# Kernel optimization log

Hardware: AMD Instinct MI355X
Metric: run time of the kernel (lower is better)

The kernel has to match this reference:

```python
import jax, jax.numpy as jnp
import numpy as np

B, NT, DIM, HEADS = 8, 16, 768, 8
RES_H = RES_W = 32
PIX = RES_H * RES_W              # 1024
CHAN_NH = 16
NH = NW = 4                      # sqrt(chan_nheads)
WH, WW = RES_H // NH, RES_W // NW  # 8, 8
HEAD_DIM = DIM // HEADS          # 96
CHAN_HEAD_DIM = PIX // CHAN_NH   # 64


def _linear(x, w, b=None):
    y = x @ w.T
    return y if b is None else y + b


def _quat_kernel(r, i, j, k):
    # Hamilton-product block kernel: (4*out_c, 4*in_c, K)
    row_r = jnp.concatenate([r, -i, -j, -k], axis=1)
    row_i = jnp.concatenate([i, r, -k, j], axis=1)
    row_j = jnp.concatenate([j, k, r, -i], axis=1)
    row_k = jnp.concatenate([k, -j, i, r], axis=1)
    return jnp.concatenate([row_r, row_i, row_j, row_k], axis=0)


def _conv1d(x, w, b=None, pad=1):
    y = jax.lax.conv_general_dilated(x, w, (1,), [(pad, pad)],
                                     dimension_numbers=('NCH', 'OIH', 'NCH'))
    return y if b is None else y + b[None, :, None]


def _win(z, t):
    # 'b t (nh h nw w) -> b (nh nw) t (h w)'
    b = z.shape[0]
    z = z.reshape(b, t, NH, WH, NW, WW).transpose(0, 2, 4, 1, 3, 5)
    return z.reshape(b, NH * NW, t, WH * WW)


def setup_inputs():
    key = jax.random.key(0)
    ks = jax.random.split(key, 24)
    s = lambda i, shape: jax.random.normal(ks[i], shape, dtype=jnp.float32) * 0.02
    return dict(
        x=jax.random.normal(ks[0], (B, PIX, DIM), jnp.float32),
        task_prompts=jax.random.normal(ks[1], (B, NT, DIM), jnp.float32),
        qkv_w=s(2, (3 * DIM, DIM)),
        proj_w=s(3, (DIM, DIM)), proj_b=s(4, (DIM,)),
        tt_w=s(5, (PIX, DIM)), tt_b=s(6, (PIX,)),
        tt1_w=s(7, (DIM, PIX)), tt1_b=s(8, (DIM,)),
        qf_r=s(9, (2, 1, 3)), qf_i=s(10, (2, 1, 3)), qf_j=s(11, (2, 1, 3)),
        qf_k=s(12, (2, 1, 3)), qf_b=s(13, (8,)),
        dqf_r=s(14, (2, 1, 3)), dqf_i=s(15, (2, 1, 3)), dqf_j=s(16, (2, 1, 3)),
        dqf_k=s(17, (2, 1, 3)), dqf_b=s(18, (4,)),
        bn_g=jnp.ones((4,), jnp.float32), bn_b=jnp.zeros((4,), jnp.float32),
        qfto_w=s(19, (1, 4, 1)),
    )


def reference(x, task_prompts, qkv_w, proj_w, proj_b, tt_w, tt_b, tt1_w, tt1_b,
              qf_r, qf_i, qf_j, qf_k, qf_b, dqf_r, dqf_i, dqf_j, dqf_k, dqf_b,
              bn_g, bn_b, qfto_w):
    # ---- spatial attention over [prompts ; pixels] ----
    xc = jnp.concatenate([task_prompts, x], axis=1)           # (B, N, C), N = NT + PIX
    b, n, c = xc.shape
    qkv = _linear(xc, qkv_w).reshape(b, n, 3, HEADS, HEAD_DIM).transpose(2, 0, 3, 1, 4)
    q, k, v = qkv[0], qkv[1], qkv[2]
    raw_spa = jnp.einsum('bhqd,bhkd->bhqk', q, k)             # pre-scale logits (returned)
    spa_attn = jax.nn.softmax(raw_spa * HEAD_DIM ** -0.5, axis=-1)
    out = jnp.einsum('bhqk,bhkd->bhqd', spa_attn, v).transpose(0, 2, 1, 3).reshape(b, n, c)
    out = _linear(out, proj_w, proj_b)
    tp_out, x_out = out[:, :-PIX, :], out[:, -PIX:, :]        # sep_prompt(x, -pixel_no)

    # ---- windowed channel attention ----
    chan_x = x[:, -PIX:, :]                                   # (B, PIX, C)
    chan_prompts = _linear(task_prompts, tt_w, tt_b)          # (B, NT, PIX)
    qw = _win(chan_prompts, NT)                               # (B, 16, NT, 64)
    kw = _win(chan_x.transpose(0, 2, 1), DIM)                 # (B, 16, C, 64)
    raw_chan = jnp.einsum('bwtd,bwcd->bwtc', qw, kw)          # (B, 16, NT, C)
    chan_attn = jax.nn.softmax(raw_chan * CHAN_HEAD_DIM ** -0.5, axis=-1)
    # chan_x output of attn@v is computed in torch but unused downstream; XLA DCEs it.
    raw_chan_r = raw_chan.reshape(b, NH, NW, NT, DIM).transpose(0, 3, 4, 1, 2)   # b t c nh nw
    chan_attn_r = chan_attn.reshape(b, NH, NW, NT, DIM).transpose(0, 3, 4, 1, 2)

    # ---- quaternion fusion of prompt streams (vectorized over the torch per-sample loop) ----
    ch_prompts = _linear(chan_prompts, tt1_w, tt1_b)          # (B, NT, C)
    zero = jnp.zeros_like(tp_out)
    quater = jnp.stack([zero, task_prompts, tp_out, ch_prompts], axis=2)  # (B, NT, 4, C)
    w1 = _quat_kernel(qf_r, qf_i, qf_j, qf_k)                 # (8, 4, 3), OIH
    fe = _conv1d(quater.reshape(b * NT, 4, DIM), w1, qf_b)    # (B*NT, 8, C)
    w2 = _quat_kernel(dqf_r, dqf_i, dqf_j, dqf_k)             # (8, 4, 3) as (in, out, K)
    w2c = jnp.flip(w2, -1).transpose(1, 0, 2)                 # conv_transpose1d(s=1,p=1) == conv1d(flip, p=K-1-1)
    fe = _conv1d(fe, w2c, dqf_b).reshape(b, NT, 4, DIM)       # (B, NT, 4, C)
    # BatchNorm1d(4) in training mode, stats per loop iteration => per-sample over (NT, C)
    mean = fe.mean(axis=(1, 3), keepdims=True)
    var = fe.var(axis=(1, 3), keepdims=True)
    fe = (fe - mean) / jnp.sqrt(var + 1e-5) * bn_g[None, None, :, None] + bn_b[None, None, :, None]
    fe = jax.nn.gelu(fe, approximate=False)
    quater_out = jnp.einsum('bnkc,k->bnc', fe, qfto_w[0, :, 0])  # Conv1d(4,1,k=1,no bias)
    return (x_out, raw_spa, spa_attn, raw_chan_r, chan_attn_r, quater_out)
```

## Files before the change

### kernel.cpp

```cpp
#include <hip/hip_runtime.h>
#include <hip/hip_bf16.h>
#include <math.h>

typedef unsigned short u16;
typedef __attribute__((ext_vector_type(8))) short  bf16x8;
typedef __attribute__((ext_vector_type(4))) float  f32x4;
typedef __attribute__((ext_vector_type(8))) u16    u16x8;
typedef __attribute__((ext_vector_type(4))) u16    u16x4;

#define B_      8
#define NT_     16
#define DIM_    768
#define HEADS_  8
#define HD_     96
#define PIX_    1024
#define NTOK_   1040
#define NPAD_   1152

#define WSO_XCB     0ull
#define WSO_WQKV    12779520ull
#define WSO_WPROJ   16318464ull
#define WSO_QB      17498112ull
#define WSO_KB      31653888ull
#define WSO_VB      45809664ull
#define WSO_VTB     59965440ull
#define WSO_ACATB   74121216ull
#define WSO_TPB     86900736ull
#define WSO_TTWB    87097344ull
#define WSO_TT1WB   88670208ull
#define WSO_CHANPB  90243072ull
#define WSO_PART    90505216ull
#define WSO_F32     95813632ull
#define FO_TPOUT    0ull
#define FO_RAWCHAN  98304ull
#define FO_CHP      1671168ull
#define FO_FE2      1769472ull
#define FO_STATS    2162688ull

#define OUT_XOUT   0ull
#define OUT_RAW    6291456ull
#define OUT_ATTN   75513856ull
#define OUT_RAWCH  144736256ull
#define OUT_ATTNCH 146309120ull
#define OUT_QOUT   147881984ull

#define SCALE_SPA 0.1020620726159658f

__device__ __forceinline__ u16 f2b(float f) {
    union { float f; unsigned u; } x; x.f = f;
    unsigned r = x.u + 0x7FFFu + ((x.u >> 16) & 1u);
    return (u16)(r >> 16);
}
__device__ __forceinline__ u16 f2b_fast(float f) {
    __hip_bfloat16 h = __float2bfloat16(f);
    return __builtin_bit_cast(u16, h);
}
__device__ __forceinline__ float b2f(u16 h) {
    union { unsigned u; float f; } x; x.u = ((unsigned)h) << 16;
    return x.f;
}

__global__ __launch_bounds__(256) void cast_concat(const float* __restrict__ tp,
                                                   const float* __restrict__ x,
                                                   u16* __restrict__ xcb) {
    size_t idx8 = ((size_t)blockIdx.x * 256 + threadIdx.x) * 8;
    int c = idx8 % DIM_;
    int n = (idx8 / DIM_) % NTOK_;
    int b = idx8 / ((size_t)DIM_ * NTOK_);
    const float* s = (n < NT_) ? tp + ((size_t)b * NT_ + n) * DIM_ + c
                               : x + ((size_t)b * PIX_ + (n - NT_)) * DIM_ + c;
    float4 a = *(const float4*)s;
    float4 d = *(const float4*)(s + 4);
    u16x8 r;
    r[0] = f2b(a.x); r[1] = f2b(a.y); r[2] = f2b(a.z); r[3] = f2b(a.w);
    r[4] = f2b(d.x); r[5] = f2b(d.y); r[6] = f2b(d.z); r[7] = f2b(d.w);
    *(u16x8*)(xcb + idx8) = r;
}

__global__ __launch_bounds__(256) void cast_all(const float* __restrict__ qkv_w,
                                                const float* __restrict__ proj_w,
                                                const float* __restrict__ tp,
                                                const float* __restrict__ tt_w,
                                                const float* __restrict__ tt1_w,
                                                u16* __restrict__ wqkvb,
                                                u16* __restrict__ wprojb,
                                                u16* __restrict__ tpb,
                                                u16* __restrict__ ttwb,
                                                u16* __restrict__ tt1wb) {
    int i = blockIdx.x * 256 + threadIdx.x;
    const float* src;
    u16* dst;
    int li;
    if (i < 221184)      { src = qkv_w;  dst = wqkvb;  li = i; }
    else if (i < 294912) { src = proj_w; dst = wprojb; li = i - 221184; }
    else if (i < 307200) { src = tp;     dst = tpb;    li = i - 294912; }
    else if (i < 405504) { src = tt_w;   dst = ttwb;   li = i - 307200; }
    else if (i < 503808) { src = tt1_w;  dst = tt1wb;  li = i - 405504; }
    else return;
    const float* s = src + (size_t)li * 8;
    float4 a = *(const float4*)s;
    float4 d = *(const float4*)(s + 4);
    u16x8 r;
    r[0] = f2b(a.x); r[1] = f2b(a.y); r[2] = f2b(a.z); r[3] = f2b(a.w);
    r[4] = f2b(d.x); r[5] = f2b(d.y); r[6] = f2b(d.z); r[7] = f2b(d.w);
    *(u16x8*)(dst + (size_t)li * 8) = r;
}

template <int MODE>
__global__ __launch_bounds__(256) void gemm_bf16(
    const u16* __restrict__ A, const u16* __restrict__ Bw,
    int lda, int ldb, int K, size_t strA, size_t strB,
    const float* __restrict__ bias,
    float* __restrict__ o0, float* __restrict__ o1,
    u16* __restrict__ oq, u16* __restrict__ ok, u16* __restrict__ ov,
    int ldo) {
    __shared__ u16 As[128][40];
    __shared__ u16 Bs[128][40];
    __shared__ float redm[128][2];
    __shared__ float reds[128][2];
    const int tid = threadIdx.x;
    const int bm = blockIdx.x, bn = blockIdx.y, z = blockIdx.z;
    const u16* Ab = A + strA * z;
    const u16* Bb = Bw + strB * z;
    const int lane = tid & 63, wid = tid >> 6;
    const int ln = lane & 15, hi = lane >> 4;
    const int wr = wid >> 1, wc = wid & 1;
    const int srow = tid >> 1, scol = (tid & 1) * 16;
    f32x4 acc[4][4] = {};
    for (int kt = 0; kt < K; kt += 32) {
        __syncthreads();
        const u16* ga = Ab + (size_t)(bm * 128 + srow) * lda + kt + scol;
        const u16* gb = Bb + (size_t)(bn * 128 + srow) * ldb + kt + scol;
        u16x8 a0 = *(const u16x8*)ga, a1 = *(const u16x8*)(ga + 8);
        u16x8 b0 = *(const u16x8*)gb, b1 = *(const u16x8*)(gb + 8);
        *(u16x8*)&As[srow][scol] = a0;
        *(u16x8*)&As[srow][scol + 8] = a1;
        *(u16x8*)&Bs[srow][scol] = b0;
        *(u16x8*)&Bs[srow][scol + 8] = b1;
        __syncthreads();
        bf16x8 af[4], bfr[4];
#pragma unroll
        for (int m = 0; m < 4; ++m) af[m] = *(const bf16x8*)&As[wr * 64 + m * 16 + ln][hi * 8];
#pragma unroll
        for (int n = 0; n < 4; ++n) bfr[n] = *(const bf16x8*)&Bs[wc * 64 + n * 16 + ln][hi * 8];
#pragma unroll
        for (int m = 0; m < 4; ++m)
#pragma unroll
            for (int n = 0; n < 4; ++n)
                acc[m][n] = __builtin_amdgcn_mfma_f32_16x16x32_bf16(af[m], bfr[n], acc[m][n], 0, 0, 0);
    }
#pragma unroll
    for (int m = 0; m < 4; ++m) {
#pragma unroll
        for (int n = 0; n < 4; ++n) {
#pragma unroll
            for (int j = 0; j < 4; ++j) {
                int gm = bm * 128 + wr * 64 + m * 16 + hi * 4 + j;
                int gn = bn * 128 + wc * 64 + n * 16 + ln;
                float v = acc[m][n][j];
                if (MODE == 0) {
                    int b = gm / NTOK_, nn = gm - b * NTOK_;
                    int s = gn / DIM_, rem = gn - s * DIM_;
                    int h = rem / HD_, d = rem - h * HD_;
                    u16 hv = f2b(v);
                    u16* dst = (s == 0) ? oq : (s == 1) ? ok : ov;
                    dst[(((size_t)b * HEADS_ + h) * NPAD_ + nn) * HD_ + d] = hv;
                } else if (MODE == 1) {
                    if (gm < NTOK_ && gn < NTOK_)
                        o0[((size_t)z * NTOK_ + gm) * NTOK_ + gn] = v;
                } else if (MODE == 2) {
                    v += bias[gn];
                    int b = gm / NTOK_, nn = gm - b * NTOK_;
                    if (nn < NT_) o1[((size_t)b * NT_ + nn) * DIM_ + gn] = v;
                    else          o0[((size_t)b * PIX_ + (nn - NT_)) * DIM_ + gn] = v;
                } else if (MODE == 3) {
                    oq[(size_t)gm * ldo + gn] = f2b(v + bias[gn]);
                } else {
                    o0[(size_t)gm * ldo + gn] = v + bias[gn];
                }
            }
        }
    }
    if (MODE == 1) {
#pragma unroll
        for (int m = 0; m < 4; ++m) {
#pragma unroll
            for (int j = 0; j < 4; ++j) {
                float v[4];
                float mx = -INFINITY;
#pragma unroll
                for (int n = 0; n < 4; ++n) {
                    int gn = bn * 128 + wc * 64 + n * 16 + ln;
                    v[n] = (gn < NTOK_) ? acc[m][n][j] * SCALE_SPA : -INFINITY;
                    mx = fmaxf(mx, v[n]);
                }
#pragma unroll
                for (int off = 1; off < 16; off <<= 1) mx = fmaxf(mx, __shfl_xor(mx, off));
                float s = 0.f;
                if (mx > -INFINITY) {
#pragma unroll
                    for (int n = 0; n < 4; ++n)
                        if (v[n] > -INFINITY) s += __expf(v[n] - mx);
                }
#pragma unroll
                for (int off = 1; off < 16; off <<= 1) s += __shfl_xor(s, off);
                if (ln == 0) {
                    int row = wr * 64 + m * 16 + hi * 4 + j;
                    redm[row][wc] = mx;
                    reds[row][wc] = s;
                }
            }
        }
        __syncthreads();
        if (tid < 128) {
            float m0 = redm[tid][0], m1 = redm[tid][1];
            float s0 = reds[tid][0], s1 = reds[tid][1];
            float M = fmaxf(m0, m1);
            float S = 0.f;
            if (m0 > -INFINITY) S += s0 * __expf(m0 - M);
            if (m1 > -INFINITY) S += s1 * __expf(m1 - M);
            float2* pp = (float2*)o1;
            pp[((size_t)z * 9 + bn) * NPAD_ + bm * 128 + tid] = make_float2(M, S);
        }
    }
}

__global__ __launch_bounds__(256) void transpose_v(const u16* __restrict__ vb,
                                                   u16* __restrict__ vtb) {
    __shared__ u16 t[32][34];
    int bi = blockIdx.x, bj = blockIdx.y, z = blockIdx.z;
    const u16* ib = vb + (size_t)z * NPAD_ * HD_;
    u16* ob = vtb + (size_t)z * HD_ * NPAD_;
    int tid = threadIdx.x;
    int r = tid >> 3, c = (tid & 7) * 4;
    *(u16x4*)&t[r][c] = *(const u16x4*)(ib + (size_t)(bi * 32 + r) * HD_ + bj * 32 + c);
    __syncthreads();
    u16x4 o;
    o[0] = t[c + 0][r]; o[1] = t[c + 1][r]; o[2] = t[c + 2][r]; o[3] = t[c + 3][r];
    *(u16x4*)(ob + (size_t)(bj * 32 + r) * NPAD_ + bi * 32 + c) = o;
}

__global__ __launch_bounds__(256) void attn_pv3(const float* __restrict__ raw,
                                                const float2* __restrict__ part,
                                                const u16* __restrict__ vtb,
                                                float* __restrict__ attn,
                                                u16* __restrict__ acat) {
    __shared__ u16 Ps[32][136];
    __shared__ float sm[32], si[32];
    const int tid = threadIdx.x;
    const int bi = blockIdx.x, z = blockIdx.y;
    if (tid < 32) {
        int grow = bi * 32 + tid;
        float M = -INFINITY;
        float mj[9], sj[9];
#pragma unroll
        for (int jt = 0; jt < 9; ++jt) {
            float2 p = part[((size_t)z * 9 + jt) * NPAD_ + grow];
            mj[jt] = p.x; sj[jt] = p.y;
            M = fmaxf(M, p.x);
        }
        float S = 0.f;
#pragma unroll
        for (int jt = 0; jt < 9; ++jt)
            if (mj[jt] > -INFINITY) S += sj[jt] * __expf(mj[jt] - M);
        sm[tid] = M;
        si[tid] = 1.f / S;
    }
    __syncthreads();
    const int lane = tid & 63, wid = tid >> 6;
    const int ln = lane & 15, hi = lane >> 4;
    const int wr = wid >> 1, wc = wid & 1;
    const int r = tid >> 3, c8 = tid & 7;
    const int grow = bi * 32 + r;
    const bool vrow = grow < NTOK_;
    const float* rp = raw + (size_t)z * NTOK_ * NTOK_ + (size_t)(vrow ? grow : 0) * NTOK_;
    float* aw = attn + (size_t)z * NTOK_ * NTOK_ + (size_t)(vrow ? grow : 0) * NTOK_;
    const u16* vbz = vtb + (size_t)z * HD_ * NPAD_;
    const float m_r = sm[r], inv_r = si[r];
    f32x4 oacc[3] = {};
    for (int c0 = 0; c0 < 1056; c0 += 128) {
        const int nsub = (c0 == 1024) ? 1 : 4;
#pragma unroll 4
        for (int s = 0; s < nsub; ++s) {
            int cl = s * 32 + c8 * 4;
            int col = c0 + cl;
            bool okc = vrow && (col < NTOK_);
            u16x4 pb = {0, 0, 0, 0};
            if (okc) {
                float4 v = *(const float4*)(rp + col);
                float4 p;
                p.x = __expf(v.x * SCALE_SPA - m_r) * inv_r;
                p.y = __expf(v.y * SCALE_SPA - m_r) * inv_r;
                p.z = __expf(v.z * SCALE_SPA - m_r) * inv_r;
                p.w = __expf(v.w * SCALE_SPA - m_r) * inv_r;
                *(float4*)(aw + col) = p;
                pb[0] = f2b_fast(p.x); pb[1] = f2b_fast(p.y);
                pb[2] = f2b_fast(p.z); pb[3] = f2b_fast(p.w);
            }
            *(u16x4*)&Ps[r][cl] = pb;
        }
        __syncthreads();
#pragma unroll 4
        for (int ktl = 0; ktl < nsub; ++ktl) {
            bf16x8 af = *(const bf16x8*)&Ps[wr * 16 + ln][ktl * 32 + hi * 8];
#pragma unroll
            for (int n = 0; n < 3; ++n) {
                bf16x8 bv = *(const bf16x8*)(vbz + (size_t)(wc * 48 + n * 16 + ln) * NPAD_
                                             + c0 + ktl * 32 + hi * 8);
                oacc[n] = __builtin_amdgcn_mfma_f32_16x16x32_bf16(af, bv, oacc[n], 0, 0, 0);
            }
        }
        __syncthreads();
    }
    const int b = z >> 3, h = z & 7;
#pragma unroll
    for (int n = 0; n < 3; ++n)
#pragma unroll
        for (int j = 0; j < 4; ++j) {
            int gi = bi * 32 + wr * 16 + hi * 4 + j;
            if (gi < NTOK_) {
                int gd = wc * 48 + n * 16 + ln;
                acat[((size_t)b * NTOK_ + gi) * DIM_ + h * HD_ + gd] = f2b(oacc[n][j]);
            }
        }
}

__global__ __launch_bounds__(256) void chan_scores(const u16* __restrict__ chanpb,
                                                   const float* __restrict__ x,
                                                   float* __restrict__ rawchan_ws,
                                                   float* __restrict__ out_raw) {
    int blk = blockIdx.x;
    int b = blk / 16, w = blk % 16;
    int cy = blockIdx.y;
    int nh = w / 4, nw = w % 4;
    __shared__ float qp[16][65];
    __shared__ float xs[64][17];
    int tid = threadIdx.x;
    for (int l = tid; l < 16 * 64; l += 256) {
        int t = l / 64, d = l % 64;
        int wh = d / 8, ww = d % 8;
        int pix = (nh * 8 + wh) * 32 + nw * 8 + ww;
        qp[t][d] = b2f(chanpb[((size_t)b * NT_ + t) * PIX_ + pix]);
    }
    __syncthreads();
    int t = tid % 16, cl = tid / 16;
    for (int cc = cy * 8; cc < cy * 8 + 8; ++cc) {
        for (int l = tid; l < 64 * 16; l += 256) {
            int d = l / 16, c2 = l % 16;
            int wh = d / 8, ww = d % 8;
            int pix = (nh * 8 + wh) * 32 + nw * 8 + ww;
            xs[d][c2] = x[((size_t)b * PIX_ + pix) * DIM_ + cc * 16 + c2];
        }
        __syncthreads();
        float acc = 0.f;
#pragma unroll
        for (int d = 0; d < 64; ++d) acc += qp[t][d] * xs[d][cl];
        int c = cc * 16 + cl;
        rawchan_ws[(((size_t)b * 16 + w) * NT_ + t) * DIM_ + c] = acc;
        out_raw[(((size_t)b * NT_ + t) * DIM_ + c) * 16 + w] = acc;
        __syncthreads();
    }
}

__global__ __launch_bounds__(256) void chan_softmax(const float* __restrict__ rawchan_ws,
                                                    float* __restrict__ out_attn) {
    int row = blockIdx.x;
    int b = row / 256;
    int w = (row / 16) % 16;
    int t = row % 16;
    const float* rp = rawchan_ws + (size_t)row * DIM_;
    int tid = threadIdx.x;
    float vals[3];
    float m = -INFINITY;
#pragma unroll
    for (int i = 0; i < 3; ++i) {
        vals[i] = rp[tid + i * 256] * 0.125f;
        m = fmaxf(m, vals[i]);
    }
    __shared__ float redm[4], reds[4];
    for (int off = 32; off; off >>= 1) m = fmaxf(m, __shfl_xor(m, off));
    if ((tid & 63) == 0) redm[tid >> 6] = m;
    __syncthreads();
    m = fmaxf(fmaxf(redm[0], redm[1]), fmaxf(redm[2], redm[3]));
    float s = 0.f;
#pragma unroll
    for (int i = 0; i < 3; ++i) { vals[i] = __expf(vals[i] - m); s += vals[i]; }
    for (int off = 32; off; off >>= 1) s += __shfl_xor(s, off);
    if ((tid & 63) == 0) reds[tid >> 6] = s;
    __syncthreads();
    s = reds[0] + reds[1] + reds[2] + reds[3];
    float inv = 1.f / s;
#pragma unroll
    for (int i = 0; i < 3; ++i) {
        int c = tid + i * 256;
        out_attn[(((size_t)b * NT_ + t) * DIM_ + c) * 16 + w] = vals[i] * inv;
    }
}

__global__ __launch_bounds__(256) void quat_conv(const float* __restrict__ tp,
                                                 const float* __restrict__ tpo,
                                                 const float* __restrict__ chp,
                                                 const float* __restrict__ qf_r, const float* __restrict__ qf_i,
                                                 const float* __restrict__ qf_j, const float* __restrict__ qf_k,
                                                 const float* __restrict__ qf_b,
                                                 const float* __restrict__ dqf_r, const float* __restrict__ dqf_i,
                                                 const float* __restrict__ dqf_j, const float* __restrict__ dqf_k,
                                                 const float* __restrict__ dqf_b,
                                                 float* __restrict__ fe2_out,
                                                 float* __restrict__ partials) {
    int blk = blockIdx.x;
    int b = blk / NT_, t = blk % NT_;
    __shared__ float w1[8][4][3];
    __shared__ float w2[8][4][3];
    __shared__ float w2c[4][8][3];
    __shared__ float qs[4][770];
    __shared__ float fs[8][770];
    __shared__ float wsum[4][4], wsq[4][4];
    int tid = threadIdx.x;
    if (tid < 96) {
        int o = tid / 12, rest = tid % 12, ic = rest / 3, tap = rest % 3;
        int g = o / 2, oo = o % 2;
        const int   cidx[4][4] = {{0, 1, 2, 3}, {1, 0, 3, 2}, {2, 3, 0, 1}, {3, 2, 1, 0}};
        const float csgn[4][4] = {{1, -1, -1, -1}, {1, 1, -1, 1}, {1, 1, 1, -1}, {1, -1, 1, 1}};
        const float* s1[4] = {qf_r, qf_i, qf_j, qf_k};
        const float* s2[4] = {dqf_r, dqf_i, dqf_j, dqf_k};
        w1[o][ic][tap] = csgn[g][ic] * s1[cidx[g][ic]][oo * 3 + tap];
        w2[o][ic][tap] = csgn[g][ic] * s2[cidx[g][ic]][oo * 3 + tap];
    }
    for (int l = tid; l < DIM_; l += 256) {
        size_t base = ((size_t)b * NT_ + t) * DIM_ + l;
        qs[0][1 + l] = 0.f;
        qs[1][1 + l] = tp[base];
        qs[2][1 + l] = tpo[base];
        qs[3][1 + l] = chp[base];
    }
    if (tid < 4) { qs[tid][0] = 0.f; qs[tid][769] = 0.f; }
    if (tid < 8) { fs[tid][0] = 0.f; fs[tid][769] = 0.f; }
    __syncthreads();
    if (tid < 96) {
        int o2 = tid / 24, rest = tid % 24, i2 = rest / 3, tap = rest % 3;
        w2c[o2][i2][tap] = w2[i2][o2][2 - tap];
    }
    for (int l = tid; l < DIM_; l += 256) {
#pragma unroll
        for (int o = 0; o < 8; ++o) {
            float a = qf_b[o];
#pragma unroll
            for (int ic = 0; ic < 4; ++ic)
#pragma unroll
                for (int tap = 0; tap < 3; ++tap) a += w1[o][ic][tap] * qs[ic][l + tap];
            fs[o][1 + l] = a;
        }
    }
    __syncthreads();
    float lsum[4] = {}, lsq[4] = {};
    for (int l = tid; l < DIM_; l += 256) {
#pragma unroll
        for (int o2 = 0; o2 < 4; ++o2) {
            float a = dqf_b[o2];
#pragma unroll
            for (int i2 = 0; i2 < 8; ++i2)
#pragma unroll
                for (int tap = 0; tap < 3; ++tap) a += w2c[o2][i2][tap] * fs[i2][l + tap];
            fe2_out[((size_t)blk * 4 + o2) * DIM_ + l] = a;
            lsum[o2] += a;
            lsq[o2] += a * a;
        }
    }
    int wid = tid >> 6;
#pragma unroll
    for (int o2 = 0; o2 < 4; ++o2) {
        float s = lsum[o2], q = lsq[o2];
        for (int off = 32; off; off >>= 1) { s += __shfl_xor(s, off); q += __shfl_xor(q, off); }
        if ((tid & 63) == 0) { wsum[wid][o2] = s; wsq[wid][o2] = q; }
    }
    __syncthreads();
    if (tid < 4) {
        float s = wsum[0][tid] + wsum[1][tid] + wsum[2][tid] + wsum[3][tid];
        float q = wsq[0][tid] + wsq[1][tid] + wsq[2][tid] + wsq[3][tid];
        partials[(size_t)blk * 8 + tid * 2 + 0] = s;
        partials[(size_t)blk * 8 + tid * 2 + 1] = q;
    }
}

__global__ __launch_bounds__(256) void bn_gelu_out(const float* __restrict__ fe2,
                                                   const float* __restrict__ partials,
                                                   const float* __restrict__ bn_g,
                                                   const float* __restrict__ bn_b,
                                                   const float* __restrict__ qfto,
                                                   float* __restrict__ out5) {
    int blk = blockIdx.x;
    int b = blk / NT_;
    int tid = threadIdx.x;
    float mean[4], rstd[4], gam[4], bet[4], qw[4];
#pragma unroll
    for (int kk = 0; kk < 4; ++kk) {
        float s = 0.f, q = 0.f;
        for (int t2 = 0; t2 < 16; ++t2) {
            const float* p = partials + ((size_t)(b * NT_ + t2) * 8 + kk * 2);
            s += p[0];
            q += p[1];
        }
        float mu = s * (1.f / 12288.f);
        float var = q * (1.f / 12288.f) - mu * mu;
        mean[kk] = mu;
        rstd[kk] = rsqrtf(var + 1e-5f);
        gam[kk] = bn_g[kk];
        bet[kk] = bn_b[kk];
        qw[kk] = qfto[kk];
    }
    for (int l = tid; l < DIM_; l += 256) {
        float acc = 0.f;
#pragma unroll
        for (int kk = 0; kk < 4; ++kk) {
            float v = fe2[((size_t)blk * 4 + kk) * DIM_ + l];
            float nrm = (v - mean[kk]) * rstd[kk] * gam[kk] + bet[kk];
            float ge = 0.5f * nrm * (1.f + erff(nrm * 0.7071067811865475f));
            acc += ge * qw[kk];
        }
        out5[(size_t)blk * DIM_ + l] = acc;
    }
}

extern "C" void kernel_launch(void* const* d_in, const int* in_sizes, int n_in,
                              void* d_out, int out_size, void* d_ws, size_t ws_size,
                              hipStream_t stream) {
    const float* x      = (const float*)d_in[0];
    const float* tp     = (const float*)d_in[1];
    const float* qkv_w  = (const float*)d_in[2];
    const float* proj_w = (const float*)d_in[3];
    const float* proj_b = (const float*)d_in[4];
    const float* tt_w   = (const float*)d_in[5];
    const float* tt_b   = (const float*)d_in[6];
    const float* tt1_w  = (const float*)d_in[7];
    const float* tt1_b  = (const float*)d_in[8];
    const float* qf_r   = (const float*)d_in[9];
    const float* qf_i   = (const float*)d_in[10];
    const float* qf_j   = (const float*)d_in[11];
    const float* qf_k   = (const float*)d_in[12];
    const float* qf_b   = (const float*)d_in[13];
    const float* dqf_r  = (const float*)d_in[14];
    const float* dqf_i  = (const float*)d_in[15];
    const float* dqf_j  = (const float*)d_in[16];
    const float* dqf_k  = (const float*)d_in[17];
    const float* dqf_b  = (const float*)d_in[18];
    const float* bn_g   = (const float*)d_in[19];
    const float* bn_b   = (const float*)d_in[20];
    const float* qfto   = (const float*)d_in[21];
    float* out = (float*)d_out;
    char* wsb = (char*)d_ws;

    u16* xcb    = (u16*)(wsb + WSO_XCB);
    u16* wqkvb  = (u16*)(wsb + WSO_WQKV);
    u16* wprojb = (u16*)(wsb + WSO_WPROJ);
    u16* qb     = (u16*)(wsb + WSO_QB);
    u16* kb     = (u16*)(wsb + WSO_KB);
    u16* vb     = (u16*)(wsb + WSO_VB);
    u16* vtb    = (u16*)(wsb + WSO_VTB);
    u16* acatb  = (u16*)(wsb + WSO_ACATB);
    u16* tpb    = (u16*)(wsb + WSO_TPB);
    u16* ttwb   = (u16*)(wsb + WSO_TTWB);
    u16* tt1wb  = (u16*)(wsb + WSO_TT1WB);
    u16* chanpb = (u16*)(wsb + WSO_CHANPB);
    float* partb = (float*)(wsb + WSO_PART);
    float* f32r = (float*)(wsb + WSO_F32);
    float* tpout   = f32r + FO_TPOUT;
    float* rawchan = f32r + FO_RAWCHAN;
    float* chpf    = f32r + FO_CHP;
    float* fe2     = f32r + FO_FE2;
    float* stats   = f32r + FO_STATS;

    cast_concat<<<3120, 256, 0, stream>>>(tp, x, xcb);
    cast_all<<<1968, 256, 0, stream>>>(qkv_w, proj_w, tp, tt_w, tt1_w,
                                       wqkvb, wprojb, tpb, ttwb, tt1wb);

    gemm_bf16<0><<<dim3(65, 18, 1), 256, 0, stream>>>(xcb, wqkvb, 768, 768, 768, 0, 0,
                                                      nullptr, nullptr, nullptr, qb, kb, vb, 0);
    transpose_v<<<dim3(36, 3, 64), 256, 0, stream>>>(vb, vtb);
    gemm_bf16<1><<<dim3(9, 9, 64), 256, 0, stream>>>(qb, kb, 96, 96, 96,
                                                     (size_t)NPAD_ * HD_, (size_t)NPAD_ * HD_,
                                                     nullptr, out + OUT_RAW, partb,
                                                     nullptr, nullptr, nullptr, 0);
    attn_pv3<<<dim3(33, 64), 256, 0, stream>>>(out + OUT_RAW, (const float2*)partb,
                                               vtb, out + OUT_ATTN, acatb);
    gemm_bf16<2><<<dim3(65, 6, 1), 256, 0, stream>>>(acatb, wprojb, 768, 768, 768, 0, 0,
                                                     proj_b, out + OUT_XOUT, tpout,
                                                     nullptr, nullptr, nullptr, 0);
    gemm_bf16<3><<<dim3(1, 8, 1), 256, 0, stream>>>(tpb, ttwb, 768, 768, 768, 0, 0,
                                                    tt_b, nullptr, nullptr, chanpb, nullptr, nullptr, 1024);
    chan_scores<<<dim3(128, 6), 256, 0, stream>>>(chanpb, x, rawchan, out + OUT_RAWCH);
    chan_softmax<<<2048, 256, 0, stream>>>(rawchan, out + OUT_ATTNCH);
    gemm_bf16<4><<<dim3(1, 6, 1), 256, 0, stream>>>(chanpb, tt1wb, 1024, 1024, 1024, 0, 0,
                                                    tt1_b, chpf, nullptr, nullptr, nullptr, nullptr, 768);
    quat_conv<<<128, 256, 0, stream>>>(tp, tpout, chpf,
                                       qf_r, qf_i, qf_j, qf_k, qf_b,
                                       dqf_r, dqf_i, dqf_j, dqf_k, dqf_b,
                                       fe2, stats);
    bn_gelu_out<<<128, 256, 0, stream>>>(fe2, stats, bn_g, bn_b, qfto, out + OUT_QOUT);
}
```

Before: 605.0 us.

## Add register-direct QK^T score kernel and reverse attn_pv3 block order

Replaces the shared-memory tiled GEMM for spatial attention scores with a dedicated kernel that loads Q and K fragments straight from global memory into registers. With head dim 96 the whole K reduction fits in registers, so the LDS staging and barriers go away. It also reverses the block index order in the following PV kernel so it starts on the most recently written score rows, which may still be in cache. The trade-off is uncoalesced per-lane global loads and no sharing of K tiles across waves.

Result: no change. 613.7 us (+1.4%).

```diff
diff --git a/kernel.cpp b/kernel.cpp
--- a/kernel.cpp
+++ b/kernel.cpp
@@ -116,8 +116,6 @@
     int ldo) {
     __shared__ u16 As[128][40];
     __shared__ u16 Bs[128][40];
-    __shared__ float redm[128][2];
-    __shared__ float reds[128][2];
     const int tid = threadIdx.x;
     const int bm = blockIdx.x, bn = blockIdx.y, z = blockIdx.z;
     const u16* Ab = A + strA * z;
@@ -165,9 +163,6 @@
                     u16 hv = f2b(v);
                     u16* dst = (s == 0) ? oq : (s == 1) ? ok : ov;
                     dst[(((size_t)b * HEADS_ + h) * NPAD_ + nn) * HD_ + d] = hv;
-                } else if (MODE == 1) {
-                    if (gm < NTOK_ && gn < NTOK_)
-                        o0[((size_t)z * NTOK_ + gm) * NTOK_ + gn] = v;
                 } else if (MODE == 2) {
                     v += bias[gn];
                     int b = gm / NTOK_, nn = gm - b * NTOK_;
@@ -181,47 +176,90 @@
             }
         }
     }
-    if (MODE == 1) {
-#pragma unroll
-        for (int m = 0; m < 4; ++m) {
+}
+
+__global__ __launch_bounds__(256) void spa_scores_direct(const u16* __restrict__ qb,
+                                                         const u16* __restrict__ kb,
+                                                         float* __restrict__ raw,
+                                                         float2* __restrict__ part) {
+    __shared__ float redm[128][2];
+    __shared__ float reds[128][2];
+    const int tid = threadIdx.x;
+    const int bm = blockIdx.x, bn = blockIdx.y, z = blockIdx.z;
+    const int lane = tid & 63, wid = tid >> 6;
+    const int ln = lane & 15, hi = lane >> 4;
+    const int wr = wid >> 1, wc = wid & 1;
+    const u16* qz = qb + (size_t)z * NPAD_ * HD_;
+    const u16* kz = kb + (size_t)z * NPAD_ * HD_;
+    bf16x8 aq[4][3];
+#pragma unroll
+    for (int m = 0; m < 4; ++m) {
+        const u16* qp_ = qz + (size_t)(bm * 128 + wr * 64 + m * 16 + ln) * HD_ + hi * 8;
+#pragma unroll
+        for (int kt = 0; kt < 3; ++kt) aq[m][kt] = *(const bf16x8*)(qp_ + kt * 32);
+    }
+    f32x4 acc[4][4] = {};
+#pragma unroll
+    for (int n = 0; n < 4; ++n) {
+        const u16* kp_ = kz + (size_t)(bn * 128 + wc * 64 + n * 16 + ln) * HD_ + hi * 8;
+        bf16x8 bk[3];
+#pragma unroll
+        for (int kt = 0; kt < 3; ++kt) bk[kt] = *(const bf16x8*)(kp_ + kt * 32);
+#pragma unroll
+        for (int kt = 0; kt < 3; ++kt)
+#pragma unroll
+            for (int m = 0; m < 4; ++m)
+                acc[m][n] = __builtin_amdgcn_mfma_f32_16x16x32_bf16(aq[m][kt], bk[kt], acc[m][n], 0, 0, 0);
+    }
+#pragma unroll
+    for (int m = 0; m < 4; ++m)
+#pragma unroll
+        for (int n = 0; n < 4; ++n)
 #pragma unroll
             for (int j = 0; j < 4; ++j) {
-                float v[4];
-                float mx = -INFINITY;
-#pragma unroll
-                for (int n = 0; n < 4; ++n) {
-                    int gn = bn * 128 + wc * 64 + n * 16 + ln;
-                    v[n] = (gn < NTOK_) ? acc[m][n][j] * SCALE_SPA : -INFINITY;
-                    mx = fmaxf(mx, v[n]);
-                }
-#pragma unroll
-                for (int off = 1; off < 16; off <<= 1) mx = fmaxf(mx, __shfl_xor(mx, off));
-                float s = 0.f;
-                if (mx > -INFINITY) {
-#pragma unroll
-                    for (int n = 0; n < 4; ++n)
-                        if (v[n] > -INFINITY) s += __expf(v[n] - mx);
-                }
-#pragma unroll
-                for (int off = 1; off < 16; off <<= 1) s += __shfl_xor(s, off);
-                if (ln == 0) {
-                    int row = wr * 64 + m * 16 + hi * 4 + j;
-                    redm[row][wc] = mx;
-                    reds[row][wc] = s;
-                }
-            }
-        }
-        __syncthreads();
-        if (tid < 128) {
-            float m0 = redm[tid][0], m1 = redm[tid][1];
-            float s0 = reds[tid][0], s1 = reds[tid][1];
-            float M = fmaxf(m0, m1);
-            float S = 0.f;
-            if (m0 > -INFINITY) S += s0 * __expf(m0 - M);
-            if (m1 > -INFINITY) S += s1 * __expf(m1 - M);
-            float2* pp = (float2*)o1;
-            pp[((size_t)z * 9 + bn) * NPAD_ + bm * 128 + tid] = make_float2(M, S);
-        }
+                int gm = bm * 128 + wr * 64 + m * 16 + hi * 4 + j;
+                int gn = bn * 128 + wc * 64 + n * 16 + ln;
+                if (gm < NTOK_ && gn < NTOK_)
+                    raw[((size_t)z * NTOK_ + gm) * NTOK_ + gn] = acc[m][n][j];
+            }
+#pragma unroll
+    for (int m = 0; m < 4; ++m) {
+#pragma unroll
+        for (int j = 0; j < 4; ++j) {
+            float v[4];
+            float mx = -INFINITY;
+#pragma unroll
+            for (int n = 0; n < 4; ++n) {
+                int gn = bn * 128 + wc * 64 + n * 16 + ln;
+                v[n] = (gn < NTOK_) ? acc[m][n][j] * SCALE_SPA : -INFINITY;
+                mx = fmaxf(mx, v[n]);
+            }
+#pragma unroll
+            for (int off = 1; off < 16; off <<= 1) mx = fmaxf(mx, __shfl_xor(mx, off));
+            float s = 0.f;
+            if (mx > -INFINITY) {
+#pragma unroll
+                for (int n = 0; n < 4; ++n)
+                    if (v[n] > -INFINITY) s += __expf(v[n] - mx);
+            }
+#pragma unroll
+            for (int off = 1; off < 16; off <<= 1) s += __shfl_xor(s, off);
+            if (ln == 0) {
+                int row = wr * 64 + m * 16 + hi * 4 + j;
+                redm[row][wc] = mx;
+                reds[row][wc] = s;
+            }
+        }
+    }
+    __syncthreads();
+    if (tid < 128) {
+        float m0 = redm[tid][0], m1 = redm[tid][1];
+        float s0 = reds[tid][0], s1 = reds[tid][1];
+        float M = fmaxf(m0, m1);
+        float S = 0.f;
+        if (m0 > -INFINITY) S += s0 * __expf(m0 - M);
+        if (m1 > -INFINITY) S += s1 * __expf(m1 - M);
+        part[((size_t)z * 9 + bn) * NPAD_ + bm * 128 + tid] = make_float2(M, S);
     }
 }
 
@@ -248,7 +286,8 @@
     __shared__ u16 Ps[32][136];
     __shared__ float sm[32], si[32];
     const int tid = threadIdx.x;
-    const int bi = blockIdx.x, z = blockIdx.y;
+    const int bi = 32 - blockIdx.x;
+    const int z  = 63 - blockIdx.y;
     if (tid < 32) {
         int grow = bi * 32 + tid;
         float M = -INFINITY;
@@ -577,10 +616,8 @@
     gemm_bf16<0><<<dim3(65, 18, 1), 256, 0, stream>>>(xcb, wqkvb, 768, 768, 768, 0, 0,
                                                       nullptr, nullptr, nullptr, qb, kb, vb, 0);
     transpose_v<<<dim3(36, 3, 64), 256, 0, stream>>>(vb, vtb);
-    gemm_bf16<1><<<dim3(9, 9, 64), 256, 0, stream>>>(qb, kb, 96, 96, 96,
-                                                     (size_t)NPAD_ * HD_, (size_t)NPAD_ * HD_,
-                                                     nullptr, out + OUT_RAW, partb,
-                                                     nullptr, nullptr, nullptr, 0);
+    spa_scores_direct<<<dim3(9, 9, 64), 256, 0, stream>>>(qb, kb, out + OUT_RAW,
+                                                          (float2*)partb);
     attn_pv3<<<dim3(33, 64), 256, 0, stream>>>(out + OUT_RAW, (const float2*)partb,
                                                vtb, out + OUT_ATTN, acatb);
     gemm_bf16<2><<<dim3(65, 6, 1), 256, 0, stream>>>(acatb, wprojb, 768, 768, 768, 0, 0,
```
